# Kernel tuning notes

Hardware: AMD Instinct MI355X
Metric: run time of the kernel (lower is better)

Reference implementation:

```python
import jax, jax.numpy as jnp
from jax import lax
import numpy as np

NUM_NODES = 30   # pinned by LayerNorm(30) in TCNBlock
H = 4            # heads
C = 64           # channel per head
HC = H * C       # 256 = all_channels, first TCN channel
F_IN = 64
B = 1024         # graphs per batch
EPG = 240        # random edges per graph (no self loops; GATv2 adds them)
LN_EPS = 1e-5
NEG_SLOPE = 0.2


def _glorot(k, shp):
    fan_in = int(np.prod(shp[1:])) if len(shp) > 1 else int(shp[0])
    return jax.random.normal(k, shp, dtype=jnp.float32) / np.sqrt(fan_in)


def setup_inputs():
    key = jax.random.key(0)
    ks = jax.random.split(key, 16)
    N = B * NUM_NODES
    # random intra-graph edges with src != dst (PyG remove_self_loops then add_self_loops)
    src_l = jax.random.randint(ks[0], (B, EPG), 0, NUM_NODES)
    off = jax.random.randint(ks[1], (B, EPG), 1, NUM_NODES)
    dst_l = (src_l + off) % NUM_NODES
    base = (jnp.arange(B) * NUM_NODES)[:, None]
    edge_index = jnp.stack([(src_l + base).reshape(-1), (dst_l + base).reshape(-1)]).astype(jnp.int32)
    z = lambda *s: jnp.zeros(s, jnp.float32)
    return {
        "x": jax.random.normal(ks[2], (N, F_IN), dtype=jnp.float32),
        "gat_Wl": _glorot(ks[3], (HC, F_IN)), "gat_bl": z(HC),
        "gat_Wr": _glorot(ks[4], (HC, F_IN)), "gat_br": z(HC),
        "gat_att": _glorot(ks[5], (H, C)), "gat_bias": z(HC),
        "tcn0_w": _glorot(ks[6], (HC, HC, 3)), "tcn0_b": z(HC),
        "ln0_w": jnp.ones((NUM_NODES,), jnp.float32), "ln0_b": z(NUM_NODES),
        "tcn1_w": _glorot(ks[7], (512, HC, 3)), "tcn1_b": z(512),
        "ln1_w": jnp.ones((NUM_NODES,), jnp.float32), "ln1_b": z(NUM_NODES),
        "ds1_w": _glorot(ks[8], (512, HC, 1)), "ds1_b": z(512),
        "tcn2_w": _glorot(ks[9], (256, 512, 3)), "tcn2_b": z(256),
        "ln2_w": jnp.ones((NUM_NODES,), jnp.float32), "ln2_b": z(NUM_NODES),
        "ds2_w": _glorot(ks[10], (256, 512, 1)), "ds2_b": z(256),
        "fc1_w": _glorot(ks[11], (512, 256 * NUM_NODES)), "fc1_b": z(512),
        "fc2_w": _glorot(ks[12], (256, 512)), "fc2_b": z(256),
        "fc3_w": _glorot(ks[13], (144, 256)), "fc3_b": z(144),
        "edge_index": edge_index,
    }


def _conv1d(x, w, b, dil):
    # torch Conv1d: x [B,Cin,L], w [Cout,Cin,K], padding = dil*(K-1)//2
    pad = dil * (w.shape[-1] - 1) // 2
    y = lax.conv_general_dilated(x, w, (1,), [(pad, pad)], rhs_dilation=(dil,),
                                 dimension_numbers=("NCH", "OIH", "NCH"))
    return y + b[None, :, None]


def _ln(x, w, b):
    # LayerNorm over last dim (length 30)
    mu = jnp.mean(x, -1, keepdims=True)
    var = jnp.var(x, -1, keepdims=True)
    return (x - mu) * lax.rsqrt(var + LN_EPS) * w + b


def reference(x, gat_Wl, gat_bl, gat_Wr, gat_br, gat_att, gat_bias,
              tcn0_w, tcn0_b, ln0_w, ln0_b,
              tcn1_w, tcn1_b, ln1_w, ln1_b, ds1_w, ds1_b,
              tcn2_w, tcn2_b, ln2_w, ln2_b, ds2_w, ds2_b,
              fc1_w, fc1_b, fc2_w, fc2_b, fc3_w, fc3_b, edge_index):
    N = x.shape[0]
    # GATv2Conv default: add self loops
    loops = jnp.arange(N, dtype=edge_index.dtype)
    ei = jnp.concatenate([edge_index, jnp.stack([loops, loops])], axis=1)
    src, dst = ei[0], ei[1]
    xl = (x @ gat_Wl.T + gat_bl).reshape(N, H, C)  # source transform
    xr = (x @ gat_Wr.T + gat_br).reshape(N, H, C)  # target transform
    s = jax.nn.leaky_relu(xl[src] + xr[dst], NEG_SLOPE)          # [E,H,C]
    e = jnp.einsum("ehc,hc->eh", s, gat_att)                     # [E,H]
    m = jax.ops.segment_max(e, dst, num_segments=N)              # segment softmax
    expe = jnp.exp(e - m[dst])
    alpha = expe / jax.ops.segment_sum(expe, dst, num_segments=N)[dst]
    agg = jax.ops.segment_sum(alpha[:, :, None] * xl[src], dst, num_segments=N)
    h = jax.nn.relu(agg.reshape(N, HC) + gat_bias)
    h = h.reshape(-1, NUM_NODES, HC).transpose(0, 2, 1)          # [B, HC, 30]
    # TCN: dilations 1,2,4; residual with 1x1 downsample when channels change
    y = jax.nn.relu(_ln(_conv1d(h, tcn0_w, tcn0_b, 1), ln0_w, ln0_b)) + h
    y = jax.nn.relu(_ln(_conv1d(y, tcn1_w, tcn1_b, 2), ln1_w, ln1_b)) + _conv1d(y, ds1_w, ds1_b, 1)
    y = jax.nn.relu(_ln(_conv1d(y, tcn2_w, tcn2_b, 4), ln2_w, ln2_b)) + _conv1d(y, ds2_w, ds2_b, 1)
    z = y.reshape(y.shape[0], -1)                                # [B, 256*30]
    z = jax.nn.relu(z @ fc1_w.T + fc1_b)
    z = jax.nn.relu(z @ fc2_w.T + fc2_b)
    out = z @ fc3_w.T + fc3_b                                    # [B, 144]
    return out, alpha, ei
```

## Files before the change

### kernel.cpp

```cpp
#include <hip/hip_runtime.h>
#include <hip/hip_bf16.h>

typedef __bf16  bf16x8 __attribute__((ext_vector_type(8)));
typedef __bf16  bf16x4 __attribute__((ext_vector_type(4)));
typedef float   f32x4  __attribute__((ext_vector_type(4)));
typedef __hip_bfloat16 bf;

__device__ __forceinline__ float clamp256(float v) {
    return fminf(fmaxf(v, -256.f), 256.f);
}
__device__ __forceinline__ float sane(float v) {
    return fminf(fmaxf(v, -1e4f), 1e4f);
}
__device__ __forceinline__ int swzk(int k, int col) {
    return (k & ~31) | ((((k >> 3) & 3) ^ ((col >> 1) & 3)) << 3) | (k & 7);
}

template<int TAPS, bool HASWD>
__global__ __launch_bounds__(256) void gemm_tf(
    const bf* __restrict__ A, const bf* __restrict__ Wt, const bf* __restrict__ Wd,
    const float* __restrict__ bias, const float* __restrict__ biasd,
    const float* __restrict__ lnw, const float* __restrict__ lnb,
    const bf* __restrict__ res, int res_stride,
    bf* __restrict__ outb, float* __restrict__ outf, int out_stride,
    int M, int N, int K, int dil, int mode, int relu, int padded, int nn, int kLen)
{
    constexpr int NT = TAPS + (HASWD ? 1 : 0);
    __shared__ __align__(16) unsigned short sA[66 * 40];
    __shared__ __align__(16) unsigned short sB[NT][64 * 40];
    __shared__ float sS[4][64], sS2[4][64];

    const int tid  = threadIdx.x;
    const int wv   = tid >> 6;
    const int lane = tid & 63;
    const int m0   = blockIdx.y * 64;
    const int n0   = blockIdx.x * 64;
    const int frow = lane & 15;
    const int fq   = lane >> 4;
    const int kOff = blockIdx.z * kLen;
    const int kEnd = (kOff + kLen < K) ? (kOff + kLen) : K;

    if (tid < 40) sA[64 * 40 + tid] = (unsigned short)0;

    int aoff[NT];
    {
        int token = wv * 16 + frow;
        int b = token >> 5, l = token & 31;
        #pragma unroll
        for (int t = 0; t < NT; ++t) {
            int s = (t < TAPS) ? (t - TAPS / 2) * dil : 0;
            int ar;
            if (padded) {
                int ls = l + s;
                ar = ((unsigned)ls < 32u) ? (b * 32 + ls) : 64;
            } else {
                ar = token;
            }
            aoff[t] = ar * 40 + fq * 8;
        }
    }

    const int srow = tid >> 2;
    const int schk = (tid & 3) << 3;
    int raG = m0 + srow;
    if (!padded && raG >= M) raG = -1;
    const int rbG  = n0 + srow;
    const bool bval = rbG < N;
    const bf* Ap = (raG >= 0) ? (A + (size_t)raG * K) : nullptr;
    const bf* Bp[NT];
    #pragma unroll
    for (int t = 0; t < NT; ++t)
        Bp[t] = (HASWD && t == TAPS) ? (Wd + (size_t)rbG * K)
                                     : (Wt + ((size_t)t * N + rbG) * K);

    f32x4 accC[4], accR[4];
    #pragma unroll
    for (int i = 0; i < 4; ++i) { accC[i] = 0.f; accR[i] = 0.f; }

    const uint4 zu = make_uint4(0u, 0u, 0u, 0u);
    uint4 pa, pb[NT];
    pa = Ap ? *(const uint4*)(Ap + kOff + schk) : zu;
    #pragma unroll
    for (int t = 0; t < NT; ++t)
        pb[t] = bval ? *(const uint4*)(Bp[t] + kOff + schk) : zu;

    for (int kb = kOff; kb < kEnd; kb += 32) {
        __syncthreads();
        *(uint4*)(sA + srow * 40 + schk) = pa;
        #pragma unroll
        for (int t = 0; t < NT; ++t)
            *(uint4*)(&sB[t][srow * 40 + schk]) = pb[t];
        __syncthreads();
        int kn = kb + 32;
        if (kn < kEnd) {
            pa = Ap ? *(const uint4*)(Ap + kn + schk) : zu;
            #pragma unroll
            for (int t = 0; t < NT; ++t)
                pb[t] = bval ? *(const uint4*)(Bp[t] + kn + schk) : zu;
        }
        #pragma unroll
        for (int t = 0; t < TAPS; ++t) {
            bf16x8 af = *(const bf16x8*)(sA + aoff[t]);
            #pragma unroll
            for (int nt = 0; nt < 4; ++nt) {
                bf16x8 bg = *(const bf16x8*)(&sB[t][(nt * 16 + frow) * 40 + fq * 8]);
                accC[nt] = __builtin_amdgcn_mfma_f32_16x16x32_bf16(af, bg, accC[nt], 0, 0, 0);
            }
        }
        if constexpr (HASWD) {
            bf16x8 af = *(const bf16x8*)(sA + aoff[TAPS]);
            #pragma unroll
            for (int nt = 0; nt < 4; ++nt) {
                bf16x8 bg = *(const bf16x8*)(&sB[TAPS][(nt * 16 + frow) * 40 + fq * 8]);
                accR[nt] = __builtin_amdgcn_mfma_f32_16x16x32_bf16(af, bg, accR[nt], 0, 0, 0);
            }
        }
    }

    if (mode == 0) {
        #pragma unroll
        for (int nt = 0; nt < 4; ++nt) {
            int col = n0 + nt * 16 + frow;
            if (col >= N) continue;
            float bv = bias ? bias[col] : 0.f;
            #pragma unroll
            for (int r = 0; r < 4; ++r) {
                int row = m0 + wv * 16 + fq * 4 + r;
                if (row >= M) continue;
                float v = accC[nt][r] + bv;
                if (relu) v = fmaxf(v, 0.f);
                if (outb) outb[(size_t)row * out_stride + col] = __float2bfloat16(clamp256(v));
                else      outf[(size_t)row * out_stride + col] = sane(v);
            }
        }
    } else if (mode == 3) {
        bf* po = outb + (size_t)blockIdx.z * M * out_stride;
        #pragma unroll
        for (int nt = 0; nt < 4; ++nt) {
            int col = n0 + nt * 16 + frow;
            if (col >= N) continue;
            #pragma unroll
            for (int r = 0; r < 4; ++r) {
                int row = m0 + wv * 16 + fq * 4 + r;
                if (row >= M) continue;
                po[(size_t)row * out_stride + col] = __float2bfloat16(accC[nt][r]);
            }
        }
    } else if (mode == 5) {
        if constexpr (HASWD) {
            bf* out2 = (bf*)res;
            int orow_[4];
            #pragma unroll
            for (int r = 0; r < 4; ++r) {
                int row = m0 + wv * 16 + fq * 4 + r;
                orow_[r] = relu ? ((row / nn) * 32 + (row % nn)) : row;
            }
            #pragma unroll
            for (int nt = 0; nt < 4; ++nt) {
                int col = n0 + nt * 16 + frow;
                if (col >= N) continue;
                float bv = bias[col], bd = biasd[col];
                #pragma unroll
                for (int r = 0; r < 4; ++r) {
                    int row = m0 + wv * 16 + fq * 4 + r;
                    if (row >= M) continue;
                    outb[(size_t)row * out_stride + col] = __float2bfloat16(clamp256(accC[nt][r] + bv));
                    out2[(size_t)orow_[r] * res_stride + col] = __float2bfloat16(clamp256(accR[nt][r] + bd));
                }
            }
        }
    } else {
        float bvc[4], bdc[4];
        #pragma unroll
        for (int nt = 0; nt < 4; ++nt) {
            int col = n0 + nt * 16 + frow;
            bvc[nt] = bias[col];
            bdc[nt] = (HASWD && biasd) ? biasd[col] : 0.f;
        }
        float s[4], s2[4];
        #pragma unroll
        for (int nt = 0; nt < 4; ++nt) { s[nt] = 0.f; s2[nt] = 0.f; }
        #pragma unroll
        for (int nt = 0; nt < 4; ++nt)
            #pragma unroll
            for (int r = 0; r < 4; ++r) {
                int row = wv * 16 + fq * 4 + r;
                int l = row & 31;
                float v = sane(accC[nt][r] + bvc[nt]);
                if (l < nn) { s[nt] += v; s2[nt] += v * v; }
            }
        #pragma unroll
        for (int nt = 0; nt < 4; ++nt) {
            s[nt]  += __shfl_xor(s[nt], 16);  s[nt]  += __shfl_xor(s[nt], 32);
            s2[nt] += __shfl_xor(s2[nt], 16); s2[nt] += __shfl_xor(s2[nt], 32);
        }
        if (fq == 0) {
            #pragma unroll
            for (int nt = 0; nt < 4; ++nt) {
                sS[wv][nt * 16 + frow]  = s[nt];
                sS2[wv][nt * 16 + frow] = s2[nt];
            }
        }
        __syncthreads();
        const int gi = wv >> 1;
        const float inv = 1.f / (float)nn;
        #pragma unroll
        for (int nt = 0; nt < 4; ++nt) {
            int c = nt * 16 + frow;
            int colg = n0 + c;
            float S  = sS[2 * gi][c]  + sS[2 * gi + 1][c];
            float S2 = sS2[2 * gi][c] + sS2[2 * gi + 1][c];
            float mu = S * inv;
            float var = S2 * inv - mu * mu;
            float rs = rsqrtf(fmaxf(var, 0.f) + 1e-5f);
            #pragma unroll
            for (int r = 0; r < 4; ++r) {
                int row = wv * 16 + fq * 4 + r;
                int l = row & 31;
                int grow = m0 + row;
                float outv = 0.f;
                if (l < nn) {
                    float v = (sane(accC[nt][r] + bvc[nt]) - mu) * rs * lnw[l] + lnb[l];
                    v = fmaxf(v, 0.f);
                    float rr;
                    if constexpr (HASWD) rr = sane(accR[nt][r] + bdc[nt]);
                    else rr = __bfloat162float(res[(size_t)grow * res_stride + colg]);
                    outv = clamp256(v + rr);
                }
                outb[(size_t)grow * out_stride + colg] = __float2bfloat16(outv);
            }
        }
    }
}

template<int TAPS, bool HASWD>
__global__ __launch_bounds__(256, 2) void gemm_tcn(
    const bf* __restrict__ A, const bf* __restrict__ Wt, const bf* __restrict__ Wd,
    const float* __restrict__ bias, const float* __restrict__ biasd,
    const float* __restrict__ lnw, const float* __restrict__ lnb,
    const bf* __restrict__ res, int res_stride,
    bf* __restrict__ outb, int out_stride,
    int M, int N, int K, int dil, int nn)
{
    constexpr int NT = TAPS + (HASWD ? 1 : 0);
    __shared__ __align__(16) unsigned short sA[257 * 40];
    __shared__ __align__(16) unsigned short sBall[2 * NT * 64 * 32];

    const int tid  = threadIdx.x;
    const int wv   = tid >> 6;
    const int lane = tid & 63;
    const int frow = lane & 15;
    const int fq   = lane >> 4;

    const int gx  = gridDim.x;
    const int nwg = gx * gridDim.y;
    int wg = blockIdx.y * gx + blockIdx.x;
    if ((nwg & 7) == 0) wg = (wg & 7) * (nwg >> 3) + (wg >> 3);
    const int n0 = (wg % gx) * 64;
    const int m0 = (wg / gx) * 256;

    if (tid < 40) sA[256 * 40 + tid] = (unsigned short)0;

    int aoff[TAPS][4];
    #pragma unroll
    for (int mr = 0; mr < 4; ++mr) {
        int token = wv * 64 + mr * 16 + frow;
        int b5 = token >> 5, l = token & 31;
        #pragma unroll
        for (int t = 0; t < TAPS; ++t) {
            int ls = l + (t - TAPS / 2) * dil;
            int ar = ((unsigned)ls < 32u) ? (b5 * 32 + ls) : 256;
            aoff[t][mr] = ar * 40 + fq * 8;
        }
    }
    const int bco = (fq ^ ((frow >> 1) & 3)) << 3;

    const int srow = tid >> 2;
    const int chS  = (tid & 3) << 3;
    const bf* Ap = A + (size_t)(m0 + srow) * K + chS;

    const bf* bsrc[4];
    {
        int lr = lane >> 2, lc = lane & 3;
        #pragma unroll
        for (int i = 0; i < 4; ++i) {
            int colb = n0 + i * 16 + lr;
            const bf* Wb;
            if (HASWD && wv == TAPS) Wb = Wd + (size_t)colb * K;
            else if (wv < TAPS)      Wb = Wt + ((size_t)wv * N + colb) * K;
            else                     Wb = Wt + (size_t)colb * K;
            bsrc[i] = Wb + lc * 8;
        }
    }

    f32x4 accC[4][4], accR[4][4];
    #pragma unroll
    for (int i = 0; i < 4; ++i)
        #pragma unroll
        for (int j = 0; j < 4; ++j) { accC[i][j] = 0.f; if (HASWD) accR[i][j] = 0.f; }

    #define ISSUE_B(BUFB, KBS)                                                      \
        if (wv < NT) {                                                              \
            unsigned short* bas = sBall + ((size_t)((BUFB) * NT + wv) * 64) * 32;   \
            _Pragma("unroll")                                                       \
            for (int i = 0; i < 4; ++i) {                                           \
                __builtin_amdgcn_global_load_lds(                                   \
                    (const __attribute__((address_space(1))) void*)(bsrc[i] + (KBS)), \
                    (__attribute__((address_space(3))) void*)(bas + i * 512),       \
                    16, 0, 0);                                                      \
            }                                                                       \
        }

    uint4 pa[4];
    #pragma unroll
    for (int i = 0; i < 4; ++i) pa[i] = *(const uint4*)(Ap + (size_t)i * 64 * K);
    ISSUE_B(0, 0);

    int buf = 0;
    for (int kb = 0; kb < K; kb += 32) {
        __syncthreads();
        #pragma unroll
        for (int i = 0; i < 4; ++i)
            *(uint4*)(sA + (srow + i * 64) * 40 + chS) = pa[i];
        __syncthreads();
        int kn = kb + 32;
        if (kn < K) {
            ISSUE_B(buf ^ 1, kn);
            #pragma unroll
            for (int i = 0; i < 4; ++i)
                pa[i] = *(const uint4*)(Ap + (size_t)i * 64 * K + kn);
        }
        const unsigned short* sBb = sBall + (size_t)buf * NT * 2048;
        bf16x8 aMid[4];
        #pragma unroll
        for (int mr = 0; mr < 4; ++mr)
            aMid[mr] = *(const bf16x8*)(sA + aoff[TAPS / 2][mr]);
        #pragma unroll
        for (int t = 0; t < TAPS; ++t) {
            bf16x8 af[4];
            #pragma unroll
            for (int mr = 0; mr < 4; ++mr)
                af[mr] = (t == TAPS / 2) ? aMid[mr]
                                         : *(const bf16x8*)(sA + aoff[t][mr]);
            #pragma unroll
            for (int nt = 0; nt < 4; ++nt) {
                bf16x8 bg = *(const bf16x8*)(sBb + (size_t)t * 2048 + (nt * 16 + frow) * 32 + bco);
                #pragma unroll
                for (int mr = 0; mr < 4; ++mr)
                    accC[mr][nt] = __builtin_amdgcn_mfma_f32_16x16x32_bf16(af[mr], bg, accC[mr][nt], 0, 0, 0);
            }
        }
        if constexpr (HASWD) {
            #pragma unroll
            for (int nt = 0; nt < 4; ++nt) {
                bf16x8 bg = *(const bf16x8*)(sBb + (size_t)TAPS * 2048 + (nt * 16 + frow) * 32 + bco);
                #pragma unroll
                for (int mr = 0; mr < 4; ++mr)
                    accR[mr][nt] = __builtin_amdgcn_mfma_f32_16x16x32_bf16(aMid[mr], bg, accR[mr][nt], 0, 0, 0);
            }
        }
        buf ^= 1;
    }
    #undef ISSUE_B

    float bvc[4], bdc[4];
    #pragma unroll
    for (int nt = 0; nt < 4; ++nt) {
        int col = n0 + nt * 16 + frow;
        bvc[nt] = bias[col];
        bdc[nt] = HASWD ? biasd[col] : 0.f;
    }
    float S[2][4], Q[2][4];
    #pragma unroll
    for (int h = 0; h < 2; ++h)
        #pragma unroll
        for (int nt = 0; nt < 4; ++nt) { S[h][nt] = 0.f; Q[h][nt] = 0.f; }
    #pragma unroll
    for (int mr = 0; mr < 4; ++mr) {
        const int h = mr >> 1;
        #pragma unroll
        for (int nt = 0; nt < 4; ++nt)
            #pragma unroll
            for (int r = 0; r < 4; ++r) {
                int l = (mr & 1) * 16 + fq * 4 + r;
                if (l < nn) {
                    float v = sane(accC[mr][nt][r] + bvc[nt]);
                    S[h][nt] += v; Q[h][nt] += v * v;
                }
            }
    }
    const float inv = 1.f / (float)nn;
    float mu[2][4], rsg[2][4];
    #pragma unroll
    for (int h = 0; h < 2; ++h)
        #pragma unroll
        for (int nt = 0; nt < 4; ++nt) {
            float s = S[h][nt], q = Q[h][nt];
            s += __shfl_xor(s, 16); s += __shfl_xor(s, 32);
            q += __shfl_xor(q, 16); q += __shfl_xor(q, 32);
            float m = s * inv;
            float var = q * inv - m * m;
            mu[h][nt]  = m;
            rsg[h][nt] = rsqrtf(fmaxf(var, 0.f) + 1e-5f);
        }
    float lw[2][4], lb2[2][4];
    #pragma unroll
    for (int p = 0; p < 2; ++p)
        #pragma unroll
        for (int r = 0; r < 4; ++r) {
            int l = p * 16 + fq * 4 + r;
            bool ok = l < nn;
            lw[p][r]  = ok ? lnw[l] : 0.f;
            lb2[p][r] = ok ? lnb[l] : 0.f;
        }
    #pragma unroll
    for (int nt = 0; nt < 4; ++nt) {
        const int colg = n0 + nt * 16 + frow;
        #pragma unroll
        for (int mr = 0; mr < 4; ++mr) {
            const int h = mr >> 1, p = mr & 1;
            #pragma unroll
            for (int r = 0; r < 4; ++r) {
                int l = p * 16 + fq * 4 + r;
                int grow = m0 + wv * 64 + mr * 16 + fq * 4 + r;
                float outv = 0.f;
                if (l < nn) {
                    float v = (sane(accC[mr][nt][r] + bvc[nt]) - mu[h][nt]) * rsg[h][nt] * lw[p][r] + lb2[p][r];
                    v = fmaxf(v, 0.f);
                    float rr;
                    if constexpr (HASWD) rr = sane(accR[mr][nt][r] + bdc[nt]);
                    else rr = __bfloat162float(res[(size_t)grow * res_stride + colg]);
                    outv = clamp256(v + rr);
                }
                outb[(size_t)grow * out_stride + colg] = __float2bfloat16(outv);
            }
        }
    }
}

#define MAXNE 270
#define XLS   260
#define SHP   264
template<int CONV>
__global__ __launch_bounds__(256, 4) void gat_fused4(
    const int* __restrict__ ei, const bf* __restrict__ xlb, const bf* __restrict__ xrb,
    const float* __restrict__ att, const float* __restrict__ gbias,
    const bf* __restrict__ Wf, const float* __restrict__ cbias,
    const float* __restrict__ lnw, const float* __restrict__ lnb,
    bf* __restrict__ yout, float* __restrict__ dalpha, float* __restrict__ dei,
    int E0, int ET, int EPG, int nn)
{
    __shared__ __align__(16) __bf16 sXL[32 * XLS];
    __shared__ __align__(16) __bf16 sHX[33 * SHP];
    __shared__ float sExp[MAXNE * 4];
    __shared__ int   sSD[MAXNE];
    __shared__ unsigned short sList[MAXNE];
    __shared__ int   sCnt[32];
    __shared__ int   sOff[33];

    const int g = blockIdx.x, tid = threadIdx.x, wv = tid >> 6, lane = tid & 63;
    if (EPG + nn > MAXNE) return;
    const int NE = EPG + nn;

    for (int k = tid; k < EPG; k += 256) {
        int s = ei[(size_t)g * EPG + k] - g * nn;
        int d = ei[(size_t)E0 + (size_t)g * EPG + k] - g * nn;
        s = min(max(s, 0), nn - 1);
        d = min(max(d, 0), nn - 1);
        sSD[k] = s | (d << 16);
    }
    for (int k = EPG + tid; k < NE; k += 256) {
        int node = k - EPG;
        sSD[k] = node | (node << 16);
    }
    {
        const uint4* gxl = (const uint4*)(xlb + (size_t)g * nn * 256);
        const uint4* gxr = (const uint4*)(xrb + (size_t)g * (CONV ? 32 : nn) * 256);
        for (int k = tid; k < nn * 32; k += 256) {
            int node = k >> 5, c8 = k & 31;
            *(uint4*)(sXL + node * XLS + c8 * 8) = gxl[k];
            *(uint4*)(sHX + k * 8) = gxr[k];
        }
    }
    if (CONV) { for (int k = tid; k < SHP; k += 256) sHX[32 * SHP + k] = (__bf16)0.f; }
    if (tid < 32) sCnt[tid] = 0;
    __syncthreads();

    for (int k = tid; k < NE; k += 256) atomicAdd(&sCnt[sSD[k] >> 16], 1);
    __syncthreads();
    if (tid < 32) {
        int acc = 0, last = 0;
        #pragma unroll
        for (int j = 0; j < 32; ++j) {
            int c = sCnt[j];
            if (j < tid) acc += c;
            if (j == 31) last = c;
        }
        sOff[tid] = acc;
        if (tid == 31) sOff[32] = acc + last;
        sCnt[tid] = 0;
    }
    __syncthreads();
    for (int k = tid; k < NE; k += 256) {
        int d = sSD[k] >> 16;
        int p = atomicAdd(&sCnt[d], 1);
        sList[sOff[d] + p] = (unsigned short)k;
    }

    for (int k = tid; k < NE; k += 256) {
        int s, d; size_t eg;
        if (k < EPG) {
            int sd = sSD[k];
            s = g * nn + (sd & 0xffff); d = g * nn + (sd >> 16);
            eg = (size_t)g * EPG + k;
        }
        else { int node = g * nn + (k - EPG); s = d = node; eg = (size_t)E0 + (size_t)g * nn + (k - EPG); }
        dei[eg] = (float)s;
        dei[(size_t)ET + eg] = (float)d;
    }
    __syncthreads();

    const float4 attv = *(const float4*)(att + lane * 4);
    const int h4 = lane >> 4;
    for (int i = wv; i < NE; i += 4) {
        int sd = sSD[i];
        int srcl = sd & 0xffff, dstl = sd >> 16;
        bf16x4 a = *(const bf16x4*)(sXL + srcl * XLS + lane * 4);
        bf16x4 b = *(const bf16x4*)(sHX + dstl * 256 + lane * 4);
        float p = 0.f;
        {
            float v0 = (float)a[0] + (float)b[0]; v0 = v0 > 0.f ? v0 : 0.2f * v0; p += v0 * attv.x;
            float v1 = (float)a[1] + (float)b[1]; v1 = v1 > 0.f ? v1 : 0.2f * v1; p += v1 * attv.y;
            float v2 = (float)a[2] + (float)b[2]; v2 = v2 > 0.f ? v2 : 0.2f * v2; p += v2 * attv.z;
            float v3 = (float)a[3] + (float)b[3]; v3 = v3 > 0.f ? v3 : 0.2f * v3; p += v3 * attv.w;
        }
        p += __shfl_xor(p, 1); p += __shfl_xor(p, 2);
        p += __shfl_xor(p, 4); p += __shfl_xor(p, 8);
        if ((lane & 15) == 0)
            sExp[i * 4 + h4] = __expf(fminf(fmaxf(p, -60.f), 60.f));
    }
    __syncthreads();

    {
        const int grp  = wv * 8 + (lane >> 3);
        const int s8   = lane & 7;
        const int chb  = s8 * 32;
        const int head = s8 >> 1;
        bf* hrow = yout + ((size_t)g * 32 + grp) * 256 + chb;

        if (grp < nn) {
            const int beg = sOff[grp], end = sOff[grp + 1];
            float den = 0.f;
            f32x4 acc[8];
            #pragma unroll
            for (int k2 = 0; k2 < 8; ++k2) acc[k2] = 0.f;

            for (int q = beg; q < end; ++q) {
                int e = sList[q];
                float ev = sExp[e * 4 + head];
                den += ev;
                const __bf16* xp = sXL + (sSD[e] & 0xffff) * XLS + chb;
                #pragma unroll
                for (int k2 = 0; k2 < 4; ++k2) {
                    bf16x8 xa = *(const bf16x8*)(xp + k2 * 8);
                    #pragma unroll
                    for (int j = 0; j < 4; ++j)
                        acc[k2 * 2][j]     += ev * (float)xa[j];
                    #pragma unroll
                    for (int j = 0; j < 4; ++j)
                        acc[k2 * 2 + 1][j] += ev * (float)xa[4 + j];
                }
            }
            const float rden = 1.f / fmaxf(den, 1e-30f);

            if (!(s8 & 1)) {
                for (int q = beg; q < end; ++q) {
                    int e = sList[q];
                    float al = fminf(fmaxf(sExp[e * 4 + head] * rden, 0.f), 1.f);
                    size_t eg = (e < EPG) ? ((size_t)g * EPG + e)
                                          : ((size_t)E0 + (size_t)g * nn + (e - EPG));
                    dalpha[eg * 4 + head] = al;
                }
            }

            #pragma unroll
            for (int k2 = 0; k2 < 8; ++k2) {
                float4 gbv = *(const float4*)(gbias + chb + k2 * 4);
                bf16x4 o;
                o[0] = (__bf16)clamp256(fmaxf(acc[k2][0] * rden + gbv.x, 0.f));
                o[1] = (__bf16)clamp256(fmaxf(acc[k2][1] * rden + gbv.y, 0.f));
                o[2] = (__bf16)clamp256(fmaxf(acc[k2][2] * rden + gbv.z, 0.f));
                o[3] = (__bf16)clamp256(fmaxf(acc[k2][3] * rden + gbv.w, 0.f));
                if constexpr (CONV) *(bf16x4*)(sHX + grp * SHP + chb + k2 * 4) = o;
                else                *(bf16x4*)(hrow + k2 * 4) = o;
            }
        } else {
            bf16x4 z; z[0] = (__bf16)0.f; z[1] = (__bf16)0.f; z[2] = (__bf16)0.f; z[3] = (__bf16)0.f;
            #pragma unroll
            for (int k2 = 0; k2 < 8; ++k2) {
                if constexpr (CONV) *(bf16x4*)(sHX + grp * SHP + chb + k2 * 4) = z;
                else                *(bf16x4*)(hrow + k2 * 4) = z;
            }
        }
    }

    if constexpr (CONV) {
        __syncthreads();
        const int frow = lane & 15;
        const int fq   = lane >> 4;
        const int colw = wv * 64;
        f32x4 c0[2][4];
        #pragma unroll
        for (int i = 0; i < 2; ++i)
            #pragma unroll
            for (int j = 0; j < 4; ++j) c0[i][j] = 0.f;

        #pragma unroll
        for (int kc = 0; kc < 8; ++kc) {
            bf16x8 af[3][2];
            #pragma unroll
            for (int t = 0; t < 3; ++t)
                #pragma unroll
                for (int mr = 0; mr < 2; ++mr) {
                    int l = mr * 16 + frow + t - 1;
                    int ar = ((unsigned)l < 32u) ? l : 32;
                    af[t][mr] = *(const bf16x8*)(sHX + ar * SHP + kc * 32 + fq * 8);
                }
            #pragma unroll
            for (int t = 0; t < 3; ++t) {
                bf16x8 bgs[4];
                #pragma unroll
                for (int nt = 0; nt < 4; ++nt) {
                    const __bf16* bp = (const __bf16*)Wf +
                        ((((size_t)(t * 16 + (colw >> 4) + nt) * 8 + kc) * 16 + frow) * 4 + fq) * 8;
                    bgs[nt] = *(const bf16x8*)bp;
                }
                #pragma unroll
                for (int nt = 0; nt < 4; ++nt) {
                    c0[0][nt] = __builtin_amdgcn_mfma_f32_16x16x32_bf16(af[t][0], bgs[nt], c0[0][nt], 0, 0, 0);
                    c0[1][nt] = __builtin_amdgcn_mfma_f32_16x16x32_bf16(af[t][1], bgs[nt], c0[1][nt], 0, 0, 0);
                }
            }
        }

        float bv[4];
        #pragma unroll
        for (int nt = 0; nt < 4; ++nt) bv[nt] = cbias[colw + nt * 16 + frow];
        float S[4], Q[4];
        #pragma unroll
        for (int nt = 0; nt < 4; ++nt) { S[nt] = 0.f; Q[nt] = 0.f; }
        #pragma unroll
        for (int mr = 0; mr < 2; ++mr)
            #pragma unroll
            for (int nt = 0; nt < 4; ++nt)
                #pragma unroll
                for (int r = 0; r < 4; ++r) {
                    int l = mr * 16 + fq * 4 + r;
                    if (l < nn) {
                        float v = sane(c0[mr][nt][r] + bv[nt]);
                        S[nt] += v; Q[nt] += v * v;
                    }
                }
        const float inv = 1.f / (float)nn;
        float mu[4], rsg[4];
        #pragma unroll
        for (int nt = 0; nt < 4; ++nt) {
            float s = S[nt], q = Q[nt];
            s += __shfl_xor(s, 16); s += __shfl_xor(s, 32);
            q += __shfl_xor(q, 16); q += __shfl_xor(q, 32);
            float m = s * inv;
            float var = q * inv - m * m;
            mu[nt]  = m;
            rsg[nt] = rsqrtf(fmaxf(var, 0.f) + 1e-5f);
        }
        float lw[2][4], lb2[2][4];
        #pragma unroll
        for (int p = 0; p < 2; ++p)
            #pragma unroll
            for (int r = 0; r < 4; ++r) {
                int l = p * 16 + fq * 4 + r;
                bool ok = l < nn;
                lw[p][r]  = ok ? lnw[l] : 0.f;
                lb2[p][r] = ok ? lnb[l] : 0.f;
            }
        #pragma unroll
        for (int nt = 0; nt < 4; ++nt) {
            const int colf = colw + nt * 16 + frow;
            #pragma unroll
            for (int mr = 0; mr < 2; ++mr)
                #pragma unroll
                for (int r = 0; r < 4; ++r) {
                    int l = mr * 16 + fq * 4 + r;
                    float outv = 0.f;
                    if (l < nn) {
                        float v = (sane(c0[mr][nt][r] + bv[nt]) - mu[nt]) * rsg[nt] * lw[mr][r] + lb2[mr][r];
                        v = fmaxf(v, 0.f);
                        float rr = (float)sHX[l * SHP + colf];
                        outv = clamp256(v + rr);
                    }
                    yout[((size_t)g * 32 + l) * 256 + colf] = __float2bfloat16(outv);
                }
        }
    }
}

struct CvtSegs { const float* in[7]; bf* out[7]; int n[7]; };
__global__ void prep_cvt(CvtSegs s, int total)
{
    int idx = blockIdx.x * 256 + threadIdx.x;
    if (idx >= total) return;
    #pragma unroll
    for (int i = 0; i < 7; ++i) {
        if (idx < s.n[i]) { s.out[i][idx] = __float2bfloat16(s.in[i][idx]); return; }
        idx -= s.n[i];
    }
}
struct TapSegs { const float* w[3]; bf* o[3]; int cc[3]; int kk[3]; int swz[3]; };
__global__ void prep_taps3(TapSegs s, int total)
{
    int idx = blockIdx.x * 256 + threadIdx.x;
    if (idx >= total) return;
    #pragma unroll
    for (int i = 0; i < 3; ++i) {
        if (idx < s.cc[i]) {
            unsigned K = (unsigned)s.kk[i];
            unsigned co = (unsigned)idx / K, ci = (unsigned)idx % K;
            int dst = co * K + (s.swz[i] ? swzk(ci, co) : ci);
            #pragma unroll
            for (int k = 0; k < 3; ++k)
                s.o[i][(size_t)k * s.cc[i] + dst] = __float2bfloat16(s.w[i][(size_t)idx * 3 + k]);
            return;
        }
        idx -= s.cc[i];
    }
}
__global__ void prep_wswz(const float* __restrict__ w, bf* __restrict__ o,
                          int total, int K, int swz)
{
    int idx = blockIdx.x * 256 + threadIdx.x;
    if (idx >= total) return;
    int co = idx / K, ci = idx % K;
    o[(size_t)co * K + (swz ? swzk(ci, co) : ci)] = __float2bfloat16(w[idx]);
}
__global__ void prep_bfrag(const float* __restrict__ w, bf* __restrict__ o, int HC)
{
    int idx = blockIdx.x * 256 + threadIdx.x;
    if (idx >= HC * HC) return;
    int co = idx / HC, ci = idx % HC;
    int cg = co >> 4, fr = co & 15, kc = ci >> 5, fq = (ci >> 3) & 3, w8 = ci & 7;
    int NCg = HC >> 4, NKc = HC >> 5;
    #pragma unroll
    for (int t = 0; t < 3; ++t) {
        size_t dst = (((((size_t)t * NCg + cg) * NKc + kc) * 16 + fr) * 4 + fq) * 8 + w8;
        o[dst] = __float2bfloat16(w[(size_t)idx * 3 + t]);
    }
}

__global__ void prep_fc1(const float* __restrict__ w, bf* __restrict__ o, int F1, int nn, int HC)
{
    int idx = blockIdx.x * 256 + threadIdx.x;
    int kw = 32 * HC;
    if (idx >= F1 * kw) return;
    int co = idx / kw, r = idx % kw, l = r / HC, ci = r % HC;
    float hv = 0.f;
    if (l < nn) hv = w[(size_t)co * (HC * nn) + ci * nn + l];
    o[idx] = __float2bfloat16(hv);
}

__global__ void fc1red(const bf* __restrict__ zp, const float* __restrict__ bias,
                       bf* __restrict__ o, int MN, int N, int S)
{
    int idx = blockIdx.x * 256 + threadIdx.x;
    if (idx >= MN) return;
    float s = 0.f;
    for (int z = 0; z < S; ++z) s += __bfloat162float(zp[(size_t)z * MN + idx]);
    o[idx] = __float2bfloat16(clamp256(fmaxf(s + bias[idx % N], 0.f)));
}

extern "C" void kernel_launch(void* const* d_in, const int* in_sizes, int n_in,
                              void* d_out, int out_size, void* d_ws, size_t ws_size,
                              hipStream_t stream)
{
    (void)n_in; (void)ws_size;
    const float* x   = (const float*)d_in[0];
    const float* Wl  = (const float*)d_in[1];  const float* bl  = (const float*)d_in[2];
    const float* Wr  = (const float*)d_in[3];  const float* br  = (const float*)d_in[4];
    const float* att = (const float*)d_in[5];  const float* gb  = (const float*)d_in[6];
    const float* t0w = (const float*)d_in[7];  const float* t0b = (const float*)d_in[8];
    const float* l0w = (const float*)d_in[9];  const float* l0b = (const float*)d_in[10];
    const float* t1w = (const float*)d_in[11]; const float* t1b = (const float*)d_in[12];
    const float* l1w = (const float*)d_in[13]; const float* l1b = (const float*)d_in[14];
    const float* d1w = (const float*)d_in[15]; const float* d1b = (const float*)d_in[16];
    const float* t2w = (const float*)d_in[17]; const float* t2b = (const float*)d_in[18];
    const float* l2w = (const float*)d_in[19]; const float* l2b = (const float*)d_in[20];
    const float* d2w = (const float*)d_in[21]; const float* d2b = (const float*)d_in[22];
    const float* f1w = (const float*)d_in[23]; const float* f1b = (const float*)d_in[24];
    const float* f2w = (const float*)d_in[25]; const float* f2b = (const float*)d_in[26];
    const float* f3w = (const float*)d_in[27]; const float* f3b = (const float*)d_in[28];
    const int*   ei  = (const int*)d_in[29];

    const int HC   = in_sizes[6];
    const int F_IN = in_sizes[1] / (HC > 0 ? HC : 1);
    const int NN   = in_sizes[0] / (F_IN > 0 ? F_IN : 1);
    const int E0   = in_sizes[29] / 2;
    const int ET   = E0 + NN;
    int nn = in_sizes[9];  nn = nn < 1 ? 1 : (nn > 32 ? 32 : nn);
    const int NG   = NN / nn;
    const int EPG  = NG > 0 ? E0 / NG : 0;
    const int C1   = in_sizes[12];
    const int C2   = in_sizes[18];
    const int F1   = in_sizes[24];
    const int F2   = in_sizes[26];
    const int F3   = in_sizes[28];
    const int NG2  = (NG + 1) / 2;

    float* dout   = (float*)d_out;
    float* dei    = dout + ((size_t)out_size - 2 * (size_t)ET);
    float* dalpha = dei - (size_t)ET * 4;

    const bool fused0 = (HC == 256) && (nn >= 1) && (nn <= 32) && (EPG + nn <= MAXNE)
                        && ((NN % 64) == 0);
    const int  gcA = NG2, gcB = NG - NG2;
    const bool fastc = ((gcA * 32) % 256 == 0) && ((gcB * 32) % 256 == 0)
                       && (C1 % 64 == 0) && (C2 % 64 == 0)
                       && (HC % 32 == 0) && (C1 % 32 == 0);

    char* ws = (char*)d_ws;
    const size_t MB = 1ull << 20;
    bf*    xb   = (bf*)(ws);
    bf*    WkA  = (bf*)(ws + 4 * MB);
    bf*    WkB  = WkA + (size_t)3 * HC * HC;
    bf*    WkC  = WkB + (size_t)3 * C1 * HC;
    bf*    Wlb  = WkC + (size_t)3 * C2 * C1;
    bf*    Wrb  = Wlb + (size_t)HC * F_IN;
    bf*    f2wb = Wrb + (size_t)HC * F_IN;
    bf*    f3wb = f2wb + (size_t)F2 * F1;
    bf*    d1wb = f3wb + (size_t)F3 * F2;
    bf*    d2wb = d1wb + (size_t)C1 * HC;
    bf*    WkAf = d2wb + (size_t)C2 * C1;
    char*  S0   = ws + (size_t)(7.5 * MB);
    char*  S1   = ws + 25 * MB;

    bf*    xrb  = (bf*)S0;
    bf*    hbuf = (bf*)S0;
    bf*    xlb  = (bf*)S1;
    bf*    y0   = fused0 ? (bf*)S0 : (bf*)S1;
    bf*    y1c  = fused0 ? (bf*)S1 : (bf*)S0;
    char*  fcS  = fused0 ? S1 : S0;
    bf*    W1t  = (bf*)fcS;
    bf*    z1p  = (bf*)(fcS + (size_t)(8.5 * MB));
    bf*    z1   = (bf*)(ws);
    bf*    z2   = (bf*)(ws + 2 * MB);

    {
        CvtSegs cs;
        cs.in[0] = x;   cs.out[0] = xb;   cs.n[0] = NN * F_IN;
        cs.in[1] = Wl;  cs.out[1] = Wlb;  cs.n[1] = HC * F_IN;
        cs.in[2] = Wr;  cs.out[2] = Wrb;  cs.n[2] = HC * F_IN;
        cs.in[3] = f2w; cs.out[3] = f2wb; cs.n[3] = F2 * F1;
        cs.in[4] = f3w; cs.out[4] = f3wb; cs.n[4] = F3 * F2;
        cs.in[5] = nullptr; cs.out[5] = nullptr; cs.n[5] = 0;
        cs.in[6] = nullptr; cs.out[6] = nullptr; cs.n[6] = 0;
        int tot = 0; for (int i = 0; i < 5; ++i) tot += cs.n[i];
        prep_cvt<<<(tot + 255) / 256, 256, 0, stream>>>(cs, tot);
        TapSegs ts;
        ts.w[0] = t0w; ts.o[0] = WkA; ts.cc[0] = HC * HC; ts.kk[0] = HC; ts.swz[0] = 0;
        ts.w[1] = t1w; ts.o[1] = WkB; ts.cc[1] = C1 * HC; ts.kk[1] = HC; ts.swz[1] = fastc ? 1 : 0;
        ts.w[2] = t2w; ts.o[2] = WkC; ts.cc[2] = C2 * C1; ts.kk[2] = C1; ts.swz[2] = fastc ? 1 : 0;
        int tt = ts.cc[0] + ts.cc[1] + ts.cc[2];
        prep_taps3<<<(tt + 255) / 256, 256, 0, stream>>>(ts, tt);
        prep_wswz<<<(C1 * HC + 255) / 256, 256, 0, stream>>>(d1w, d1wb, C1 * HC, HC, fastc ? 1 : 0);
        prep_wswz<<<(C2 * C1 + 255) / 256, 256, 0, stream>>>(d2w, d2wb, C2 * C1, C1, fastc ? 1 : 0);
        if (fused0)
            prep_bfrag<<<(HC * HC + 255) / 256, 256, 0, stream>>>(t0w, WkAf, HC);
    }

    gemm_tf<1, true><<<dim3((HC + 63) / 64, (NN + 63) / 64), 256, 0, stream>>>(
        xb, Wlb, Wrb, bl, br, nullptr, nullptr, (const bf*)xrb, HC,
        xlb, nullptr, HC, NN, HC, F_IN, 1, 5, fused0 ? 1 : 0, 0, nn, F_IN);

    if (fused0)
        gat_fused4<1><<<NG, 256, 0, stream>>>(ei, xlb, xrb, att, gb,
                                              WkAf, t0b, l0w, l0b,
                                              y0, dalpha, dei, E0, ET, EPG, nn);
    else {
        gat_fused4<0><<<NG, 256, 0, stream>>>(ei, xlb, xrb, att, gb,
                                              nullptr, nullptr, nullptr, nullptr,
                                              hbuf, dalpha, dei, E0, ET, EPG, nn);
        gemm_tf<3, false><<<dim3((HC + 63) / 64, NG * 32 / 64), 256, 0, stream>>>(
            hbuf, WkA, nullptr, t0b, nullptr, l0w, l0b, hbuf, HC,
            y0, nullptr, HC, NG * 32, HC, HC, 1, 2, 0, 1, nn, HC);
    }

    for (int c = 0; c < 2; ++c) {
        int g0 = c * NG2;
        int gc = (c == 0) ? NG2 : (NG - NG2);
        if (gc <= 0) continue;
        const bf* y0c = y0 + (size_t)g0 * 32 * HC;
        bf*       y2c = y0 + (size_t)g0 * 32 * HC;
        if (fastc) {
            gemm_tcn<3, true><<<dim3(C1 / 64, gc * 32 / 256), 256, 0, stream>>>(
                y0c, WkB, d1wb, t1b, d1b, l1w, l1b, nullptr, 0,
                y1c, C1, gc * 32, C1, HC, 2, nn);
            gemm_tcn<3, true><<<dim3(C2 / 64, gc * 32 / 256), 256, 0, stream>>>(
                y1c, WkC, d2wb, t2b, d2b, l2w, l2b, nullptr, 0,
                y2c, C2, gc * 32, C2, C1, 4, nn);
        } else {
            gemm_tf<3, true><<<dim3((C1 + 63) / 64, gc * 32 / 64), 256, 0, stream>>>(
                y0c, WkB, d1wb, t1b, d1b, l1w, l1b, nullptr, 0,
                y1c, nullptr, C1, gc * 32, C1, HC, 2, 2, 0, 1, nn, HC);
            gemm_tf<3, true><<<dim3((C2 + 63) / 64, gc * 32 / 64), 256, 0, stream>>>(
                y1c, WkC, d2wb, t2b, d2b, l2w, l2b, nullptr, 0,
                y2c, nullptr, C2, gc * 32, C2, C1, 4, 2, 0, 1, nn, C1);
        }
    }

    prep_fc1<<<(F1 * 32 * HC + 255) / 256, 256, 0, stream>>>(f1w, W1t, F1, nn, HC);
    gemm_tf<1, false><<<dim3((F1 + 63) / 64, (NG + 63) / 64, 8), 256, 0, stream>>>(
        y0, W1t, nullptr, nullptr, nullptr, nullptr, nullptr, nullptr, 0,
        z1p, nullptr, F1, NG, F1, 32 * HC, 1, 3, 0, 0, nn, 4 * HC);
    fc1red<<<(NG * F1 + 255) / 256, 256, 0, stream>>>(z1p, f1b, z1, NG * F1, F1, 8);

    gemm_tf<1, false><<<dim3((F2 + 63) / 64, (NG + 63) / 64), 256, 0, stream>>>(
        z1, f2wb, nullptr, f2b, nullptr, nullptr, nullptr, nullptr, 0,
        z2, nullptr, F2, NG, F2, F1, 1, 0, 1, 0, nn, F1);
    gemm_tf<1, false><<<dim3((F3 + 63) / 64, (NG + 63) / 64), 256, 0, stream>>>(
        z2, f3wb, nullptr, f3b, nullptr, nullptr, nullptr, nullptr, 0,
        nullptr, dout, F3, NG, F3, F2, 1, 0, 0, 0, nn, F2);
}
```

Before: 498.7 us.

## Replace CSR edge aggregation with dense per-graph attention matrix MFMA

Drops the per-destination CSR build (atomic counting, prefix scan, list fill) and the scalar per-edge weighted accumulation in the GAT kernel. Each block now scatters exp scores into a dense 4x32x33 attention matrix in shared memory, normalizes rows to get softmax denominators and alpha, and computes the aggregation as a bf16 MFMA product of the 32x32 per-head matrix with the node features. The matrix shares LDS with the xr/conv buffer. This adds shared-memory float atomics, strided scalar B-fragment loads, and bf16 rounding of attention weights before aggregation.

```diff
diff --git a/kernel.cpp b/kernel.cpp
--- a/kernel.cpp
+++ b/kernel.cpp
@@ -442,7 +442,7 @@
 #define XLS   260
 #define SHP   264
 template<int CONV>
-__global__ __launch_bounds__(256, 4) void gat_fused4(
+__global__ __launch_bounds__(256, 4) void gat_fused5(
     const int* __restrict__ ei, const bf* __restrict__ xlb, const bf* __restrict__ xrb,
     const float* __restrict__ att, const float* __restrict__ gbias,
     const bf* __restrict__ Wf, const float* __restrict__ cbias,
@@ -451,16 +451,16 @@
     int E0, int ET, int EPG, int nn)
 {
     __shared__ __align__(16) __bf16 sXL[32 * XLS];
-    __shared__ __align__(16) __bf16 sHX[33 * SHP];
+    __shared__ __align__(16) float sPH[(33 * SHP) / 2];
     __shared__ float sExp[MAXNE * 4];
     __shared__ int   sSD[MAXNE];
-    __shared__ unsigned short sList[MAXNE];
-    __shared__ int   sCnt[32];
-    __shared__ int   sOff[33];
+    __shared__ float sDen[128];
 
     const int g = blockIdx.x, tid = threadIdx.x, wv = tid >> 6, lane = tid & 63;
     if (EPG + nn > MAXNE) return;
     const int NE = EPG + nn;
+    __bf16* sHX = (__bf16*)sPH;
+    __bf16* Pb  = (__bf16*)sPH;
 
     for (int k = tid; k < EPG; k += 256) {
         int s = ei[(size_t)g * EPG + k] - g * nn;
@@ -481,31 +481,12 @@
             *(uint4*)(sXL + node * XLS + c8 * 8) = gxl[k];
             *(uint4*)(sHX + k * 8) = gxr[k];
         }
-    }
-    if (CONV) { for (int k = tid; k < SHP; k += 256) sHX[32 * SHP + k] = (__bf16)0.f; }
-    if (tid < 32) sCnt[tid] = 0;
+        const uint4 zu = make_uint4(0u, 0u, 0u, 0u);
+        for (int k = nn * 32 + tid; k < 32 * 32; k += 256)
+            *(uint4*)(sXL + (k >> 5) * XLS + (k & 31) * 8) = zu;
+    }
+    if (CONV) { __bf16 z = (__bf16)0.f; for (int k = tid; k < SHP; k += 256) sHX[32 * SHP + k] = z; }
     __syncthreads();
-
-    for (int k = tid; k < NE; k += 256) atomicAdd(&sCnt[sSD[k] >> 16], 1);
-    __syncthreads();
-    if (tid < 32) {
-        int acc = 0, last = 0;
-        #pragma unroll
-        for (int j = 0; j < 32; ++j) {
-            int c = sCnt[j];
-            if (j < tid) acc += c;
-            if (j == 31) last = c;
-        }
-        sOff[tid] = acc;
-        if (tid == 31) sOff[32] = acc + last;
-        sCnt[tid] = 0;
-    }
-    __syncthreads();
-    for (int k = tid; k < NE; k += 256) {
-        int d = sSD[k] >> 16;
-        int p = atomicAdd(&sCnt[d], 1);
-        sList[sOff[d] + p] = (unsigned short)k;
-    }
 
     for (int k = tid; k < NE; k += 256) {
         int s, d; size_t eg;
@@ -518,7 +499,6 @@
         dei[eg] = (float)s;
         dei[(size_t)ET + eg] = (float)d;
     }
-    __syncthreads();
 
     const float4 attv = *(const float4*)(att + lane * 4);
     const int h4 = lane >> 4;
@@ -541,73 +521,99 @@
     }
     __syncthreads();
 
+    for (int k = tid; k < 4 * 32 * 33; k += 256) sPH[k] = 0.f;
+    __syncthreads();
+
+    for (int k = tid; k < NE; k += 256) {
+        int sd = sSD[k];
+        int s = sd & 0xffff, d = sd >> 16;
+        int base = d * 33 + s;
+        #pragma unroll
+        for (int h = 0; h < 4; ++h)
+            atomicAdd(&sPH[h * 1056 + base], sExp[k * 4 + h]);
+    }
+    __syncthreads();
+
+    const int prow = tid >> 1;
+    const int phalf = tid & 1;
+    float pv[16];
     {
-        const int grp  = wv * 8 + (lane >> 3);
-        const int s8   = lane & 7;
-        const int chb  = s8 * 32;
-        const int head = s8 >> 1;
-        bf* hrow = yout + ((size_t)g * 32 + grp) * 256 + chb;
-
-        if (grp < nn) {
-            const int beg = sOff[grp], end = sOff[grp + 1];
-            float den = 0.f;
-            f32x4 acc[8];
-            #pragma unroll
-            for (int k2 = 0; k2 < 8; ++k2) acc[k2] = 0.f;
-
-            for (int q = beg; q < end; ++q) {
-                int e = sList[q];
-                float ev = sExp[e * 4 + head];
-                den += ev;
-                const __bf16* xp = sXL + (sSD[e] & 0xffff) * XLS + chb;
-                #pragma unroll
-                for (int k2 = 0; k2 < 4; ++k2) {
-                    bf16x8 xa = *(const bf16x8*)(xp + k2 * 8);
-                    #pragma unroll
-                    for (int j = 0; j < 4; ++j)
-                        acc[k2 * 2][j]     += ev * (float)xa[j];
-                    #pragma unroll
-                    for (int j = 0; j < 4; ++j)
-                        acc[k2 * 2 + 1][j] += ev * (float)xa[4 + j];
-                }
-            }
-            const float rden = 1.f / fmaxf(den, 1e-30f);
-
-            if (!(s8 & 1)) {
-                for (int q = beg; q < end; ++q) {
-                    int e = sList[q];
-                    float al = fminf(fmaxf(sExp[e * 4 + head] * rden, 0.f), 1.f);
-                    size_t eg = (e < EPG) ? ((size_t)g * EPG + e)
-                                          : ((size_t)E0 + (size_t)g * nn + (e - EPG));
-                    dalpha[eg * 4 + head] = al;
-                }
-            }
-
-            #pragma unroll
-            for (int k2 = 0; k2 < 8; ++k2) {
-                float4 gbv = *(const float4*)(gbias + chb + k2 * 4);
-                bf16x4 o;
-                o[0] = (__bf16)clamp256(fmaxf(acc[k2][0] * rden + gbv.x, 0.f));
-                o[1] = (__bf16)clamp256(fmaxf(acc[k2][1] * rden + gbv.y, 0.f));
-                o[2] = (__bf16)clamp256(fmaxf(acc[k2][2] * rden + gbv.z, 0.f));
-                o[3] = (__bf16)clamp256(fmaxf(acc[k2][3] * rden + gbv.w, 0.f));
-                if constexpr (CONV) *(bf16x4*)(sHX + grp * SHP + chb + k2 * 4) = o;
-                else                *(bf16x4*)(hrow + k2 * 4) = o;
-            }
-        } else {
-            bf16x4 z; z[0] = (__bf16)0.f; z[1] = (__bf16)0.f; z[2] = (__bf16)0.f; z[3] = (__bf16)0.f;
-            #pragma unroll
-            for (int k2 = 0; k2 < 8; ++k2) {
-                if constexpr (CONV) *(bf16x4*)(sHX + grp * SHP + chb + k2 * 4) = z;
-                else                *(bf16x4*)(hrow + k2 * 4) = z;
-            }
-        }
+        const float* pr = sPH + prow * 33 + phalf * 16;
+        #pragma unroll
+        for (int j = 0; j < 16; ++j) pv[j] = pr[j];
+        float ssum = 0.f;
+        #pragma unroll
+        for (int j = 0; j < 16; ++j) ssum += pv[j];
+        ssum += __shfl_xor(ssum, 1);
+        if (!phalf) sDen[prow] = ssum;
+    }
+    __syncthreads();
+
+    for (int k = tid; k < NE; k += 256) {
+        int d = sSD[k] >> 16;
+        size_t eg = (k < EPG) ? ((size_t)g * EPG + k)
+                              : ((size_t)E0 + (size_t)g * nn + (k - EPG));
+        #pragma unroll
+        for (int h = 0; h < 4; ++h) {
+            float rd = 1.f / fmaxf(sDen[h * 32 + d], 1e-30f);
+            dalpha[eg * 4 + h] = fminf(fmaxf(sExp[k * 4 + h] * rd, 0.f), 1.f);
+        }
+    }
+    {
+        float rd = 1.f / fmaxf(sDen[prow], 1e-30f);
+        bf16x8 w0, w1;
+        #pragma unroll
+        for (int j = 0; j < 8; ++j) w0[j] = (__bf16)(pv[j] * rd);
+        #pragma unroll
+        for (int j = 0; j < 8; ++j) w1[j] = (__bf16)(pv[8 + j] * rd);
+        __bf16* pw = Pb + prow * 40 + phalf * 16;
+        *(bf16x8*)(pw)     = w0;
+        *(bf16x8*)(pw + 8) = w1;
+    }
+    __syncthreads();
+
+    const int frow = lane & 15;
+    const int fq   = lane >> 4;
+    f32x4 hacc[2][4];
+    #pragma unroll
+    for (int dt = 0; dt < 2; ++dt)
+        #pragma unroll
+        for (int ct = 0; ct < 4; ++ct) hacc[dt][ct] = 0.f;
+    {
+        bf16x8 afr[2];
+        #pragma unroll
+        for (int dt = 0; dt < 2; ++dt)
+            afr[dt] = *(const bf16x8*)(Pb + (wv * 32 + dt * 16 + frow) * 40 + fq * 8);
+        #pragma unroll
+        for (int ct = 0; ct < 4; ++ct) {
+            const int chc = wv * 64 + ct * 16 + frow;
+            bf16x8 bfr;
+            #pragma unroll
+            for (int s2 = 0; s2 < 8; ++s2)
+                bfr[s2] = sXL[(fq * 8 + s2) * XLS + chc];
+            hacc[0][ct] = __builtin_amdgcn_mfma_f32_16x16x32_bf16(afr[0], bfr, hacc[0][ct], 0, 0, 0);
+            hacc[1][ct] = __builtin_amdgcn_mfma_f32_16x16x32_bf16(afr[1], bfr, hacc[1][ct], 0, 0, 0);
+        }
+    }
+    __syncthreads();
+
+    #pragma unroll
+    for (int ct = 0; ct < 4; ++ct) {
+        const int ch = wv * 64 + ct * 16 + frow;
+        const float gb = gbias[ch];
+        #pragma unroll
+        for (int dt = 0; dt < 2; ++dt)
+            #pragma unroll
+            for (int r = 0; r < 4; ++r) {
+                int d = dt * 16 + fq * 4 + r;
+                float v = (d < nn) ? clamp256(fmaxf(hacc[dt][ct][r] + gb, 0.f)) : 0.f;
+                if constexpr (CONV) sHX[d * SHP + ch] = (__bf16)v;
+                else yout[((size_t)g * 32 + d) * 256 + ch] = __float2bfloat16(v);
+            }
     }
 
     if constexpr (CONV) {
         __syncthreads();
-        const int frow = lane & 15;
-        const int fq   = lane >> 4;
         const int colw = wv * 64;
         f32x4 c0[2][4];
         #pragma unroll
@@ -880,11 +886,11 @@
         xlb, nullptr, HC, NN, HC, F_IN, 1, 5, fused0 ? 1 : 0, 0, nn, F_IN);
 
     if (fused0)
-        gat_fused4<1><<<NG, 256, 0, stream>>>(ei, xlb, xrb, att, gb,
+        gat_fused5<1><<<NG, 256, 0, stream>>>(ei, xlb, xrb, att, gb,
                                               WkAf, t0b, l0w, l0b,
                                               y0, dalpha, dei, E0, ET, EPG, nn);
     else {
-        gat_fused4<0><<<NG, 256, 0, stream>>>(ei, xlb, xrb, att, gb,
+        gat_fused5<0><<<NG, 256, 0, stream>>>(ei, xlb, xrb, att, gb,
                                               nullptr, nullptr, nullptr, nullptr,
                                               hbuf, dalpha, dei, E0, ET, EPG, nn);
         gemm_tf<3, false><<<dim3((HC + 63) / 64, NG * 32 / 64), 256, 0, stream>>>(
```

Result: no change. 496.5 us (-0.4%).
